# Performance work log

Measured on AMD Instinct MI355X. Metric: run time of the kernel, lower is better.

Reference implementation:

```python
import jax, jax.numpy as jnp
import numpy as np

N_POINTS = 131072
NUM_FREQS = 6
MIN_LOG2_FREQ = 0.0
MAX_LOG2_FREQ = 5.0
NUM_QUANTS = 80
NUM_FEATS = 4
NUM_CORRS = 8
STD = 1e-4


def setup_inputs() -> dict:
    key = jax.random.key(0)
    k1, k2 = jax.random.split(key)
    # points in [-1, 1] as typical normalized NeRF scene coordinates
    points = jax.random.uniform(k1, (N_POINTS, 3), jnp.float32, -1.0, 1.0)
    # QFF1.__init__: std ** (1/x_dim), qff_vector ~ randn * std'
    std = STD ** (1.0 / 3.0)
    qff_vector = jax.random.normal(
        k2, (NUM_FREQS * 2 * 3, NUM_FEATS * NUM_CORRS, NUM_QUANTS, 1), jnp.float32) * std
    freqs = (2.0 ** jnp.linspace(MIN_LOG2_FREQ, MAX_LOG2_FREQ, NUM_FREQS)).astype(jnp.float32)
    return {"points": points, "qff_vector": qff_vector, "freqs": freqs}


def _lerp_lookup(qv, enc):
    # 1D linear interpolation, equivalent to F.grid_sample(bilinear, align_corners=True)
    # on a (Q, 1) grid with x coord fixed to 0.
    # qv: (M, CR, Q) tables; enc: (M, N) coords in [-1, 1].
    Q = qv.shape[-1]
    pos = (enc + 1.0) * 0.5 * (Q - 1)            # (M, N) in [0, Q-1]
    i0 = jnp.clip(jnp.floor(pos), 0, Q - 1).astype(jnp.int32)
    i1 = jnp.minimum(i0 + 1, Q - 1)
    w = (pos - i0.astype(pos.dtype))[:, None, :]  # (M, 1, N)
    gather = jax.vmap(lambda q, i: q[:, i])       # per-row gather: (CR, Q), (N) -> (CR, N)
    v0 = gather(qv, i0)                           # (M, CR, N)
    v1 = gather(qv, i1)
    return v0 * (1.0 - w) + v1 * w


def reference(points, qff_vector, freqs):
    # points: (N, 3); qff_vector: (NF*2*3, C*R, Q, 1); freqs: (NF,)
    N = points.shape[0]
    NF = freqs.shape[0]
    CR, Q = qff_vector.shape[1], qff_vector.shape[2]
    R = NUM_CORRS
    C = CR // R
    # pos_encode: (NF, 3, N) -> stack sin/cos -> (NF*2*3, N)
    fp = points.T[None, :, :] * freqs[:, None, None]
    enc = jnp.stack((jnp.sin(fp), jnp.cos(fp)), 1).reshape(NF * 2 * 3, N)
    qv = qff_vector.reshape(NF * 2 * 3, CR, Q)
    sampled = _lerp_lookup(qv, enc)               # (NF*2*3, C*R, N)
    sampled = sampled.reshape(NF * 2, 3, C, R, N)
    # CP decomposition: product over the 3 axes, sum over rank R
    f = (sampled[:, 0] * sampled[:, 1] * sampled[:, 2]).sum(2)  # (NF*2, C, N)
    return f.reshape(NF * 2 * C, N).T             # (N, latent_dim=NF*2*C)
```

## Files before the change

kernel.cpp:

```cpp
#include <hip/hip_runtime.h>
#include <hip/hip_fp16.h>
#include <math.h>


constexpr int N_POINTS = 131072;
constexpr int NFREQ    = 6;
constexpr int QN       = 80;
constexpr int CRN      = 32;
constexpr int M_PER_F  = 6;
constexpr int ROW      = 40;
constexpr int MSTRIDE  = QN * ROW;
constexpr int TSTRIDE  = CRN * QN;
constexpr int FH       = M_PER_F * MSTRIDE;
constexpr int FH4      = FH / 8;
constexpr int NTAB     = NFREQ * M_PER_F;
constexpr int TB       = 512;
constexpr int PPB      = 256;
constexpr int NBLK     = N_POINTS / PPB;
constexpr int DSTR     = 25;
constexpr size_t TAB_BYTES = (size_t)NTAB * MSTRIDE * 2;

typedef float f32x4 __attribute__((ext_vector_type(4)));

__global__ __launch_bounds__(256)
void qff1_prep(const float* __restrict__ qff, __half* __restrict__ wsh)
{
    int i = blockIdx.x * 256 + threadIdx.x;
    if (i >= NTAB * TSTRIDE) return;
    int T  = i / TSTRIDE;
    int r  = i - T * TSTRIDE;
    int cr = r / QN;
    int q  = r - cr * QN;
    wsh[T * MSTRIDE + q * ROW + cr] = __float2half(qff[i]);
}

__global__ __launch_bounds__(TB, 2)
void qff1_main(const float* __restrict__ points,
               const __half* __restrict__ wsh,
               const float* __restrict__ freqs,
               float4* __restrict__ out4)
{
    __shared__ __align__(16) __half  tab[FH];
    __shared__ __align__(16) __half2 dmp2[PPB * DSTR];

    const int tid = threadIdx.x;
    const int p   = tid & (PPB - 1);
    const int h   = tid >> 8;
    const int n   = blockIdx.x * PPB + p;

    const float px = points[n * 3 + 0];
    const float py = points[n * 3 + 1];
    const float pz = points[n * 3 + 2];

    for (int f = 0; f < NFREQ; ++f) {
        {
            const float4* src = reinterpret_cast<const float4*>(wsh + (size_t)f * FH);
            float4* dst = reinterpret_cast<float4*>(tab);
#pragma unroll
            for (int k = 0; k < 5; ++k) {
                int idx = tid + k * TB;
                if (idx < FH4) dst[idx] = src[idx];
            }
        }
        __syncthreads();

        const float freq = freqs[f];

        float ee[3];
        {
            float s0, c0, s1, c1, s2, c2;
            __sincosf(px * freq, &s0, &c0);
            __sincosf(py * freq, &s1, &c1);
            __sincosf(pz * freq, &s2, &c2);
            ee[0] = h ? c0 : s0;
            ee[1] = h ? c1 : s1;
            ee[2] = h ? c2 : s2;
        }

        int b0[3], b1[3];
        __half2 w2[3];
#pragma unroll
        for (int d = 0; d < 3; ++d) {
            float pos = (ee[d] + 1.0f) * (0.5f * (float)(QN - 1));
            float fi  = floorf(pos);
            int i0    = (int)fi;
            i0 = i0 < 0 ? 0 : (i0 > QN - 1 ? QN - 1 : i0);
            int i1 = i0 + 1; if (i1 > QN - 1) i1 = QN - 1;
            w2[d] = __float2half2_rn(pos - (float)i0);
            int m = h * 3 + d;
            b0[d] = m * MSTRIDE + i0 * ROW;
            b1[d] = m * MSTRIDE + i1 * ROW;
        }

        float acc[4];
#pragma unroll
        for (int jc = 0; jc < 4; ++jc) {
            __half2 Lv[3][4];
#pragma unroll
            for (int d = 0; d < 3; ++d) {
                union { float4 v; __half2 hh[4]; } A, B;
                A.v = *(const float4*)&tab[b0[d] + jc * 8];
                B.v = *(const float4*)&tab[b1[d] + jc * 8];
#pragma unroll
                for (int kk = 0; kk < 4; ++kk)
                    Lv[d][kk] = __hfma2(w2[d], __hsub2(B.hh[kk], A.hh[kk]), A.hh[kk]);
            }
            float a = 0.0f;
#pragma unroll
            for (int kk = 0; kk < 4; ++kk) {
                float2 f0 = __half22float2(Lv[0][kk]);
                float2 f1 = __half22float2(Lv[1][kk]);
                float2 f2 = __half22float2(Lv[2][kk]);
                a += f0.x * f1.x * f2.x + f0.y * f1.y * f2.y;
            }
            acc[jc] = a;
        }

        dmp2[p * DSTR + h * 12 + f * 2 + 0] = __floats2half2_rn(acc[0], acc[1]);
        dmp2[p * DSTR + h * 12 + f * 2 + 1] = __floats2half2_rn(acc[2], acc[3]);

        __syncthreads();
    }

    const size_t base = (size_t)blockIdx.x * (PPB * 12);
#pragma unroll
    for (int k = 0; k < 6; ++k) {
        int i  = tid + k * TB;
        int pp = i / 12;
        int c  = i - pp * 12;
        int off = (c & 1) * 12 + (c >> 1) * 2;
        float2 lo = __half22float2(dmp2[pp * DSTR + off + 0]);
        float2 hi = __half22float2(dmp2[pp * DSTR + off + 1]);
        f32x4 v = { lo.x, lo.y, hi.x, hi.y };
        __builtin_nontemporal_store(v, (f32x4*)&out4[base + i]);
    }
}

__global__ __launch_bounds__(512, 8)
void qff1_fallback(const float* __restrict__ points,
                   const float* __restrict__ qff,
                   const float* __restrict__ freqs,
                   float* __restrict__ out)
{
    __shared__ __align__(16) __half tab[FH];
    const int tid = threadIdx.x;
    const int f   = blockIdx.y;

    const float* tsrc = qff + (size_t)f * (M_PER_F * CRN * QN);
    __half2* lds2 = reinterpret_cast<__half2*>(tab);
    for (int idx = tid; idx < M_PER_F * QN * (CRN / 2); idx += 512) {
        int m   = idx / (QN * CRN / 2);
        int rem = idx - m * (QN * CRN / 2);
        int q   = rem >> 4;
        int cr2 = rem & 15;
        float v0 = tsrc[m * (CRN * QN) + (2 * cr2    ) * QN + q];
        float v1 = tsrc[m * (CRN * QN) + (2 * cr2 + 1) * QN + q];
        lds2[m * (MSTRIDE / 2) + q * (ROW / 2) + cr2] = __floats2half2_rn(v0, v1);
    }
    __syncthreads();

    const int n = blockIdx.x * 512 + tid;
    const float px = points[n * 3 + 0];
    const float py = points[n * 3 + 1];
    const float pz = points[n * 3 + 2];
    const float freq = freqs[f];

    float enc[6];
    {
        float s, cc;
        __sincosf(px * freq, &s, &cc); enc[0] = s; enc[3] = cc;
        __sincosf(py * freq, &s, &cc); enc[1] = s; enc[4] = cc;
        __sincosf(pz * freq, &s, &cc); enc[2] = s; enc[5] = cc;
    }
    int b0[6], b1[6];
    __half2 w2[6];
#pragma unroll
    for (int m = 0; m < 6; ++m) {
        float pos = (enc[m] + 1.0f) * (0.5f * (float)(QN - 1));
        float fi  = floorf(pos);
        int i0    = (int)fi;
        i0 = i0 < 0 ? 0 : (i0 > QN - 1 ? QN - 1 : i0);
        int i1 = i0 + 1; if (i1 > QN - 1) i1 = QN - 1;
        w2[m] = __float2half2_rn(pos - (float)i0);
        b0[m] = m * MSTRIDE + i0 * ROW;
        b1[m] = m * MSTRIDE + i1 * ROW;
    }
    float accv[8];
#pragma unroll
    for (int s = 0; s < 2; ++s) {
#pragma unroll
        for (int jc = 0; jc < 4; ++jc) {
            __half2 Lv[3][4];
#pragma unroll
            for (int d = 0; d < 3; ++d) {
                int m = s * 3 + d;
                union { float4 v; __half2 hh[4]; } A, B;
                A.v = *(const float4*)&tab[b0[m] + jc * 8];
                B.v = *(const float4*)&tab[b1[m] + jc * 8];
#pragma unroll
                for (int kk = 0; kk < 4; ++kk)
                    Lv[d][kk] = __hfma2(w2[m], __hsub2(B.hh[kk], A.hh[kk]), A.hh[kk]);
            }
            float a = 0.0f;
#pragma unroll
            for (int kk = 0; kk < 4; ++kk) {
                float2 f0 = __half22float2(Lv[0][kk]);
                float2 f1 = __half22float2(Lv[1][kk]);
                float2 f2 = __half22float2(Lv[2][kk]);
                a += f0.x * f1.x * f2.x + f0.y * f1.y * f2.y;
            }
            accv[s * 4 + jc] = a;
        }
    }
    float4* o = (float4*)(out + (size_t)n * 48 + f * 8);
    o[0] = make_float4(accv[0], accv[1], accv[2], accv[3]);
    o[1] = make_float4(accv[4], accv[5], accv[6], accv[7]);
}

extern "C" void kernel_launch(void* const* d_in, const int* in_sizes, int n_in,
                              void* d_out, int out_size, void* d_ws, size_t ws_size,
                              hipStream_t stream) {
    const float* points = (const float*)d_in[0];
    const float* qff    = (const float*)d_in[1];
    const float* freqs  = (const float*)d_in[2];
    float* out = (float*)d_out;

    if (ws_size >= TAB_BYTES) {
        __half* wsh = (__half*)d_ws;
        qff1_prep<<<dim3((NTAB * TSTRIDE + 255) / 256), dim3(256), 0, stream>>>(qff, wsh);
        qff1_main<<<dim3(NBLK), dim3(TB), 0, stream>>>(points, wsh, freqs, (float4*)out);
    } else {
        qff1_fallback<<<dim3(N_POINTS / 512, NFREQ), dim3(512), 0, stream>>>(points, qff, freqs, out);
    }
}
```

Baseline: 33.25 us.

## Double-buffer per-frequency LDS tables and enlarge blocks to 1024 threads

The main kernel now holds two LDS table buffers. While the current frequency's lookups run, it loads the next frequency's table from global memory into registers and writes it to the other buffer. This removes the load-then-sync stall at the start of each frequency iteration. Block size is doubled to 1024 threads handling 512 points, so total LDS per block grows to about 125KB, which allows only one block per CU. The tighter launch-bounds hint and the extra prefetch registers risk register spills.

```diff
diff --git a/kernel.cpp b/kernel.cpp
--- a/kernel.cpp
+++ b/kernel.cpp
@@ -14,8 +14,8 @@
 constexpr int FH       = M_PER_F * MSTRIDE;
 constexpr int FH4      = FH / 8;
 constexpr int NTAB     = NFREQ * M_PER_F;
-constexpr int TB       = 512;
-constexpr int PPB      = 256;
+constexpr int TB       = 1024;
+constexpr int PPB      = 512;
 constexpr int NBLK     = N_POINTS / PPB;
 constexpr int DSTR     = 25;
 constexpr size_t TAB_BYTES = (size_t)NTAB * MSTRIDE * 2;
@@ -34,38 +34,51 @@
     wsh[T * MSTRIDE + q * ROW + cr] = __float2half(qff[i]);
 }
 
-__global__ __launch_bounds__(TB, 2)
+__global__ __launch_bounds__(TB, 4)
 void qff1_main(const float* __restrict__ points,
                const __half* __restrict__ wsh,
                const float* __restrict__ freqs,
                float4* __restrict__ out4)
 {
-    __shared__ __align__(16) __half  tab[FH];
+    __shared__ __align__(16) __half  tabA[FH];
+    __shared__ __align__(16) __half  tabB[FH];
     __shared__ __align__(16) __half2 dmp2[PPB * DSTR];
 
     const int tid = threadIdx.x;
     const int p   = tid & (PPB - 1);
-    const int h   = tid >> 8;
+    const int h   = tid >> 9;
     const int n   = blockIdx.x * PPB + p;
 
     const float px = points[n * 3 + 0];
     const float py = points[n * 3 + 1];
     const float pz = points[n * 3 + 2];
 
+    const int i0 = tid, i1 = tid + TB, i2 = tid + 2 * TB;
+
+    {
+        const float4* src = reinterpret_cast<const float4*>(wsh);
+        float4* dst = reinterpret_cast<float4*>(tabA);
+        dst[i0] = src[i0];
+        dst[i1] = src[i1];
+        if (i2 < FH4) dst[i2] = src[i2];
+    }
+    __syncthreads();
+
     for (int f = 0; f < NFREQ; ++f) {
-        {
-            const float4* src = reinterpret_cast<const float4*>(wsh + (size_t)f * FH);
-            float4* dst = reinterpret_cast<float4*>(tab);
-#pragma unroll
-            for (int k = 0; k < 5; ++k) {
-                int idx = tid + k * TB;
-                if (idx < FH4) dst[idx] = src[idx];
-            }
-        }
-        __syncthreads();
+        const __half* cur = (f & 1) ? tabB : tabA;
+        float4* nxt = reinterpret_cast<float4*>((f & 1) ? tabA : tabB);
+        const bool more = (f + 1 < NFREQ);
+
+        float4 sv0, sv1, sv2;
+        if (more) {
+            const float4* src =
+                reinterpret_cast<const float4*>(wsh + (size_t)(f + 1) * FH);
+            sv0 = src[i0];
+            sv1 = src[i1];
+            if (i2 < FH4) sv2 = src[i2];
+        }
 
         const float freq = freqs[f];
-
         float ee[3];
         {
             float s0, c0, s1, c1, s2, c2;
@@ -83,13 +96,13 @@
         for (int d = 0; d < 3; ++d) {
             float pos = (ee[d] + 1.0f) * (0.5f * (float)(QN - 1));
             float fi  = floorf(pos);
-            int i0    = (int)fi;
-            i0 = i0 < 0 ? 0 : (i0 > QN - 1 ? QN - 1 : i0);
-            int i1 = i0 + 1; if (i1 > QN - 1) i1 = QN - 1;
-            w2[d] = __float2half2_rn(pos - (float)i0);
+            int q0    = (int)fi;
+            q0 = q0 < 0 ? 0 : (q0 > QN - 1 ? QN - 1 : q0);
+            int q1 = q0 + 1; if (q1 > QN - 1) q1 = QN - 1;
+            w2[d] = __float2half2_rn(pos - (float)q0);
             int m = h * 3 + d;
-            b0[d] = m * MSTRIDE + i0 * ROW;
-            b1[d] = m * MSTRIDE + i1 * ROW;
+            b0[d] = m * MSTRIDE + q0 * ROW;
+            b1[d] = m * MSTRIDE + q1 * ROW;
         }
 
         float acc[4];
@@ -99,8 +112,8 @@
 #pragma unroll
             for (int d = 0; d < 3; ++d) {
                 union { float4 v; __half2 hh[4]; } A, B;
-                A.v = *(const float4*)&tab[b0[d] + jc * 8];
-                B.v = *(const float4*)&tab[b1[d] + jc * 8];
+                A.v = *(const float4*)&cur[b0[d] + jc * 8];
+                B.v = *(const float4*)&cur[b1[d] + jc * 8];
 #pragma unroll
                 for (int kk = 0; kk < 4; ++kk)
                     Lv[d][kk] = __hfma2(w2[d], __hsub2(B.hh[kk], A.hh[kk]), A.hh[kk]);
@@ -119,6 +132,11 @@
         dmp2[p * DSTR + h * 12 + f * 2 + 0] = __floats2half2_rn(acc[0], acc[1]);
         dmp2[p * DSTR + h * 12 + f * 2 + 1] = __floats2half2_rn(acc[2], acc[3]);
 
+        if (more) {
+            nxt[i0] = sv0;
+            nxt[i1] = sv1;
+            if (i2 < FH4) nxt[i2] = sv2;
+        }
         __syncthreads();
     }
 
@@ -178,12 +196,12 @@
     for (int m = 0; m < 6; ++m) {
         float pos = (enc[m] + 1.0f) * (0.5f * (float)(QN - 1));
         float fi  = floorf(pos);
-        int i0    = (int)fi;
-        i0 = i0 < 0 ? 0 : (i0 > QN - 1 ? QN - 1 : i0);
-        int i1 = i0 + 1; if (i1 > QN - 1) i1 = QN - 1;
-        w2[m] = __float2half2_rn(pos - (float)i0);
-        b0[m] = m * MSTRIDE + i0 * ROW;
-        b1[m] = m * MSTRIDE + i1 * ROW;
+        int q0    = (int)fi;
+        q0 = q0 < 0 ? 0 : (q0 > QN - 1 ? QN - 1 : q0);
+        int q1 = q0 + 1; if (q1 > QN - 1) q1 = QN - 1;
+        w2[m] = __float2half2_rn(pos - (float)q0);
+        b0[m] = m * MSTRIDE + q0 * ROW;
+        b1[m] = m * MSTRIDE + q1 * ROW;
     }
     float accv[8];
 #pragma unroll
```

After: 32.34 us. 1.03x faster.
